# Kernel tuning notes

Measured on AMD Instinct MI355X. Metric: run time of the kernel, lower is better.

## Reference

```python
import jax, jax.numpy as jnp
import numpy as np

# Morphological dilation (max-plus "convolution"), per-channel:
#   out[b,y,x,c] = max_{i,j} ( x_padded[b, y+i, x+j, c] + w[i, j, c] )
# TF SAME padding for k=4, stride 1: pad_total=3 -> pad_before=1, pad_after=2.
# Out-of-bounds positions act as -inf (identity for max), matching tf.nn.dilation2d.

def setup_inputs() -> dict:
    key = jax.random.key(0)
    kx, kw = jax.random.split(key)
    x = jax.random.normal(kx, (8, 512, 512, 32), dtype=jnp.float32)
    w = jax.random.normal(kw, (4, 4, 32), dtype=jnp.float32) * 0.1
    return {"x": x, "w": w}


def reference(x, w):
    kh, kw_ = w.shape[0], w.shape[1]
    H, W = x.shape[1], x.shape[2]
    pt, pl = (kh - 1) // 2, (kw_ - 1) // 2          # pad before (TF SAME)
    pb, pr = kh - 1 - pt, kw_ - 1 - pl              # pad after
    xp = jnp.pad(x, ((0, 0), (pt, pb), (pl, pr), (0, 0)),
                 constant_values=-jnp.inf)
    out = jnp.full(x.shape, -jnp.inf, dtype=x.dtype)
    # Small fixed kh*kw loop (16 iters); each iter is a fused shift+add+max.
    for i in range(kh):
        for j in range(kw_):
            out = jnp.maximum(out, xp[:, i:i + H, j:j + W, :] + w[i, j])
    return out
```

## Files before the change

### kernel.cpp

```cpp
#include <hip/hip_runtime.h>
#include <math.h>


constexpr int H = 512;
constexpr int W = 512;
constexpr int C = 32;
constexpr int CHUNK = 128;

template<int P, bool STORE, bool XEDGE>
__device__ __forceinline__ void step(const float* __restrict__ xb,
                                     float* __restrict__ ob,
                                     const float wv[16], float acc[4],
                                     const int yy, const int xp) {
    constexpr int S0 = P;
    constexpr int S1 = (P + 1) & 3;
    constexpr int S2 = (P + 2) & 3;
    constexpr int S3 = (P + 3) & 3;
    const float NI = -INFINITY;

    const bool yok = ((unsigned)yy < (unsigned)H);
    const int  yc  = min(max(yy, 0), H - 1);
    const float* rowp = xb + (size_t)yc * (W * C);

    float px[4];
#pragma unroll
    for (int j = 0; j < 4; ++j) {
        int xx = xp + j - 1;
        bool ok = yok;
        if (XEDGE) {
            ok = ok & ((unsigned)xx < (unsigned)W);
            xx = min(max(xx, 0), W - 1);
        }
        float v = rowp[(size_t)xx * C];
        px[j] = ok ? v : NI;
    }

    acc[S1] = fmaxf(acc[S1], fmaxf(fmaxf(px[0] + wv[ 0], px[1] + wv[ 1]),
                                   fmaxf(px[2] + wv[ 2], px[3] + wv[ 3])));
    acc[S0] = fmaxf(acc[S0], fmaxf(fmaxf(px[0] + wv[ 4], px[1] + wv[ 5]),
                                   fmaxf(px[2] + wv[ 6], px[3] + wv[ 7])));
    acc[S3] = fmaxf(acc[S3], fmaxf(fmaxf(px[0] + wv[ 8], px[1] + wv[ 9]),
                                   fmaxf(px[2] + wv[10], px[3] + wv[11])));
    acc[S2] = fmaxf(acc[S2], fmaxf(fmaxf(px[0] + wv[12], px[1] + wv[13]),
                                   fmaxf(px[2] + wv[14], px[3] + wv[15])));

    if (STORE)
        __builtin_nontemporal_store(acc[S2], ob + (size_t)(yy - 2) * (W * C));
    acc[S2] = NI;
}

template<bool XEDGE>
__device__ __forceinline__ void chunk_body(const float* __restrict__ xb,
                                           float* __restrict__ ob,
                                           const float wv[16], float acc[4],
                                           const int y0, const int xp) {
    step<3, false, XEDGE>(xb, ob, wv, acc, y0 - 1, xp);
    step<0, false, XEDGE>(xb, ob, wv, acc, y0,     xp);
    step<1, false, XEDGE>(xb, ob, wv, acc, y0 + 1, xp);
    for (int s = 0; s < CHUNK; s += 4) {
        const int yy = y0 + 2 + s;
        step<2, true, XEDGE>(xb, ob, wv, acc, yy,     xp);
        step<3, true, XEDGE>(xb, ob, wv, acc, yy + 1, xp);
        step<0, true, XEDGE>(xb, ob, wv, acc, yy + 2, xp);
        step<1, true, XEDGE>(xb, ob, wv, acc, yy + 3, xp);
    }
}

__global__ __launch_bounds__(256)
void dil2d_kernel(const float* __restrict__ xin,
                  const float* __restrict__ wt,
                  float* __restrict__ out) {
    const int c  = threadIdx.x & (C - 1);
    const int xl = threadIdx.x >> 5;
    const int xp = blockIdx.x * 8 + xl;
    const int y0 = blockIdx.y * CHUNK;
    const int b  = blockIdx.z;

    float wv[16];
#pragma unroll
    for (int k = 0; k < 16; ++k)
        wv[k] = wt[k * C + c];

    float acc[4] = { -INFINITY, -INFINITY, -INFINITY, -INFINITY };

    const float* xb = xin + (size_t)b * H * W * C + c;
    float* ob = out + ((size_t)b * H * W + xp) * C + c;

    const bool xedge = (blockIdx.x == 0) || (blockIdx.x == gridDim.x - 1);
    if (xedge) chunk_body<true >(xb, ob, wv, acc, y0, xp);
    else       chunk_body<false>(xb, ob, wv, acc, y0, xp);
}

extern "C" void kernel_launch(void* const* d_in, const int* in_sizes, int n_in,
                              void* d_out, int out_size, void* d_ws, size_t ws_size,
                              hipStream_t stream) {
    const float* x = (const float*)d_in[0];
    const float* w = (const float*)d_in[1];
    float* o = (float*)d_out;

    dim3 block(256);
    dim3 grid(W / 8,
              H / CHUNK,
              8);
    dil2d_kernel<<<grid, block, 0, stream>>>(x, w, o);
}
```

Before: 103.1 us.

## Batch row loads ahead of accumulation and halve row chunk size

Splits each row step into a separate load phase and accumulate phase, so all 16 loads of a 4-row group are issued before any max-plus arithmetic runs. This raises memory-level parallelism per thread. The row chunk per block also drops from 128 to 64, doubling the grid for better occupancy and load balance, at the cost of more redundant halo rows (3 extra per 64) and more registers held for the batched loads.

```diff
diff --git a/kernel.cpp b/kernel.cpp
--- a/kernel.cpp
+++ b/kernel.cpp
@@ -5,24 +5,16 @@
 constexpr int H = 512;
 constexpr int W = 512;
 constexpr int C = 32;
-constexpr int CHUNK = 128;
+constexpr int CHUNK = 64;
 
-template<int P, bool STORE, bool XEDGE>
-__device__ __forceinline__ void step(const float* __restrict__ xb,
-                                     float* __restrict__ ob,
-                                     const float wv[16], float acc[4],
-                                     const int yy, const int xp) {
-    constexpr int S0 = P;
-    constexpr int S1 = (P + 1) & 3;
-    constexpr int S2 = (P + 2) & 3;
-    constexpr int S3 = (P + 3) & 3;
+template<bool XEDGE>
+__device__ __forceinline__ void load_row(const float* __restrict__ xb,
+                                         const int yy, const int xp,
+                                         float px[4]) {
     const float NI = -INFINITY;
-
     const bool yok = ((unsigned)yy < (unsigned)H);
     const int  yc  = min(max(yy, 0), H - 1);
     const float* rowp = xb + (size_t)yc * (W * C);
-
-    float px[4];
 #pragma unroll
     for (int j = 0; j < 4; ++j) {
         int xx = xp + j - 1;
@@ -34,6 +26,16 @@
         float v = rowp[(size_t)xx * C];
         px[j] = ok ? v : NI;
     }
+}
+
+template<int P, bool STORE>
+__device__ __forceinline__ void accum(float* __restrict__ ob,
+                                      const float wv[16], float acc[4],
+                                      const float px[4], const int yy) {
+    constexpr int S0 = P;
+    constexpr int S1 = (P + 1) & 3;
+    constexpr int S2 = (P + 2) & 3;
+    constexpr int S3 = (P + 3) & 3;
 
     acc[S1] = fmaxf(acc[S1], fmaxf(fmaxf(px[0] + wv[ 0], px[1] + wv[ 1]),
                                    fmaxf(px[2] + wv[ 2], px[3] + wv[ 3])));
@@ -46,7 +48,7 @@
 
     if (STORE)
         __builtin_nontemporal_store(acc[S2], ob + (size_t)(yy - 2) * (W * C));
-    acc[S2] = NI;
+    acc[S2] = -INFINITY;
 }
 
 template<bool XEDGE>
@@ -54,15 +56,26 @@
                                            float* __restrict__ ob,
                                            const float wv[16], float acc[4],
                                            const int y0, const int xp) {
-    step<3, false, XEDGE>(xb, ob, wv, acc, y0 - 1, xp);
-    step<0, false, XEDGE>(xb, ob, wv, acc, y0,     xp);
-    step<1, false, XEDGE>(xb, ob, wv, acc, y0 + 1, xp);
+    {
+        float p0[4], p1[4], p2[4];
+        load_row<XEDGE>(xb, y0 - 1, xp, p0);
+        load_row<XEDGE>(xb, y0,     xp, p1);
+        load_row<XEDGE>(xb, y0 + 1, xp, p2);
+        accum<3, false>(ob, wv, acc, p0, y0 - 1);
+        accum<0, false>(ob, wv, acc, p1, y0);
+        accum<1, false>(ob, wv, acc, p2, y0 + 1);
+    }
     for (int s = 0; s < CHUNK; s += 4) {
         const int yy = y0 + 2 + s;
-        step<2, true, XEDGE>(xb, ob, wv, acc, yy,     xp);
-        step<3, true, XEDGE>(xb, ob, wv, acc, yy + 1, xp);
-        step<0, true, XEDGE>(xb, ob, wv, acc, yy + 2, xp);
-        step<1, true, XEDGE>(xb, ob, wv, acc, yy + 3, xp);
+        float p0[4], p1[4], p2[4], p3[4];
+        load_row<XEDGE>(xb, yy,     xp, p0);
+        load_row<XEDGE>(xb, yy + 1, xp, p1);
+        load_row<XEDGE>(xb, yy + 2, xp, p2);
+        load_row<XEDGE>(xb, yy + 3, xp, p3);
+        accum<2, true>(ob, wv, acc, p0, yy);
+        accum<3, true>(ob, wv, acc, p1, yy + 1);
+        accum<0, true>(ob, wv, acc, p2, yy + 2);
+        accum<1, true>(ob, wv, acc, p3, yy + 3);
     }
 }
 
```

Measured after the change: 106.7 us. 1.03x slower.
